# Optimization experiments

Measured on AMD Instinct MI355X. Metric: run time of the kernel, lower is better.

## Reference

```python
import jax, jax.numpy as jnp
import numpy as np
import math

N_VERT = 35709
N_FACE = 70789
BATCH = 32


def _normalize(x, axis=-1, eps=1e-12):
    n = jnp.linalg.norm(x, axis=axis, keepdims=True)
    return x / jnp.maximum(n, eps)


def setup_inputs() -> dict:
    key = jax.random.key(0)
    ks = jax.random.split(key, 9)
    coeff = jax.random.normal(ks[0], (BATCH, 277), jnp.float32)
    idBase = jax.random.normal(ks[1], (3 * N_VERT, 80), jnp.float32)
    exBase = jax.random.normal(ks[2], (3 * N_VERT, 64), jnp.float32)
    texBase = jax.random.normal(ks[3], (3 * N_VERT, 100), jnp.float32)
    meanshape = jax.random.normal(ks[4], (3 * N_VERT,), jnp.float32)
    meantex = jax.random.normal(ks[5], (3 * N_VERT,), jnp.float32)
    face_buf = jax.random.randint(ks[6], (N_FACE, 3), 0, N_VERT, jnp.int32)
    # point_buf may index the appended zero-normal row at position N_FACE (padding)
    point_buf = jax.random.randint(ks[7], (N_VERT, 8), 0, N_FACE + 1, jnp.int32)
    keypoints = jax.random.randint(ks[8], (68,), 0, N_VERT, jnp.int32)
    return dict(coeff=coeff, idBase=idBase, exBase=exBase, texBase=texBase,
                meanshape=meanshape, meantex=meantex, face_buf=face_buf,
                point_buf=point_buf, keypoints=keypoints)


def reference(coeff, idBase, exBase, texBase, meanshape, meantex,
              face_buf, point_buf, keypoints):
    B = coeff.shape[0]
    # ---- Split_coeff (canonical 80/64/100/3/27/3 layout) ----
    id_c = coeff[:, :80]
    ex_c = coeff[:, 80:144]
    tex_c = coeff[:, 144:244]
    angles = coeff[:, 244:247]
    gamma = coeff[:, 247:274]
    trans = coeff[:, 274:277]
    cam_scale = jnp.ones((B, 1), coeff.dtype)
    f_scale = jnp.ones((B, 1), coeff.dtype)

    # ---- Shape formation ----
    fs = (jnp.einsum('ij,aj->ai', idBase, id_c)
          + jnp.einsum('ij,aj->ai', exBase, ex_c)
          + meanshape[None, :])
    fs = fs.reshape(B, -1, 3)  # [B, N, 3]
    fs = fs - jnp.mean(meanshape.reshape(-1, 3), axis=0)[None, None, :]

    # ---- Texture formation ----
    tex = (jnp.einsum('ij,aj->ai', texBase, tex_c) + meantex[None, :]).reshape(B, -1, 3)

    # ---- Rotation matrix (Rz @ Ry @ Rx, then transpose) ----
    cx, sx = jnp.cos(angles[:, 0]), jnp.sin(angles[:, 0])
    cy, sy = jnp.cos(angles[:, 1]), jnp.sin(angles[:, 1])
    cz, sz = jnp.cos(angles[:, 2]), jnp.sin(angles[:, 2])
    o, z = jnp.ones_like(cx), jnp.zeros_like(cx)
    Rx = jnp.stack([o, z, z, z, cx, -sx, z, sx, cx], -1).reshape(B, 3, 3)
    Ry = jnp.stack([cy, z, sy, z, o, z, -sy, z, cy], -1).reshape(B, 3, 3)
    Rz = jnp.stack([cz, -sz, z, sz, cz, z, z, z, o], -1).reshape(B, 3, 3)
    rot = jnp.swapaxes(jnp.matmul(jnp.matmul(Rz, Ry), Rx), 1, 2)  # [B,3,3]

    # ---- Compute_norm: gather face verts, cross, aggregate to vertices ----
    v1 = fs[:, face_buf[:, 0], :]  # [B, F, 3]
    v2 = fs[:, face_buf[:, 1], :]
    v3 = fs[:, face_buf[:, 2], :]
    face_norm = _normalize(jnp.cross(v1 - v2, v2 - v3), axis=2)  # [B, F, 3]
    face_norm = jnp.concatenate(
        [face_norm, jnp.zeros((B, 1, 3), face_norm.dtype)], axis=1)  # pad row
    v_norm = _normalize(jnp.sum(face_norm[:, point_buf, :], axis=2), axis=2)  # [B,N,3]

    norm_r = jnp.matmul(v_norm, rot)

    # ---- Rigid transform + landmarks ----
    fst = jnp.matmul(fs, rot) + trans[:, None, :]
    lm = fst[:, keypoints, :]  # [B, 68, 3]

    # ---- Projection block (applied to landmarks) ----
    focal = 1015.0 * f_scale  # [B,1]
    camera_pos = jnp.array([0.0, 0.0, 10.0], coeff.dtype) * cam_scale[:, :, None]  # [B,1,3]
    reverse_z = jnp.diag(jnp.array([1.0, 1.0, -1.0], coeff.dtype))
    z1 = jnp.zeros((B, 1), coeff.dtype)
    z2 = jnp.zeros((B, 2), coeff.dtype)
    o1 = jnp.ones((B, 1), coeff.dtype)
    p_matrix = jnp.concatenate(
        [focal, z1, 112.0 * o1, z1, focal, 112.0 * o1, z2, o1], axis=1).reshape(B, 3, 3)
    lm_cam = jnp.matmul(lm, reverse_z[None]) + camera_pos
    aug = jnp.matmul(lm_cam, jnp.swapaxes(p_matrix, 1, 2))
    landmark_p = aug[..., :2] / aug[..., 2:3]

    # ---- SH illumination ----
    init_lit = jnp.array([0.8, 0, 0, 0, 0, 0, 0, 0, 0], coeff.dtype)
    g = gamma.reshape(B, 3, 9) + init_lit[None, None, :]
    pi = math.pi
    a0, a1, a2 = pi, 2 * pi / math.sqrt(3.0), 2 * pi / math.sqrt(8.0)
    c0 = 1.0 / math.sqrt(4 * pi)
    c1 = math.sqrt(3.0) / math.sqrt(4 * pi)
    c2 = 3 * math.sqrt(5.0) / math.sqrt(12 * pi)
    nx, ny, nz = norm_r[..., 0], norm_r[..., 1], norm_r[..., 2]
    Y = jnp.stack([
        a0 * c0 * jnp.ones_like(nx),
        -a1 * c1 * ny,
        a1 * c1 * nz,
        -a1 * c1 * nx,
        a2 * c2 * nx * ny,
        -a2 * c2 * ny * nz,
        a2 * c2 * 0.5 / math.sqrt(3.0) * (3 * nz * nz - 1),
        -a2 * c2 * nx * nz,
        a2 * c2 * 0.5 * (nx * nx - ny * ny),
    ], axis=-1)  # [B, N, 9]
    lighting = jnp.einsum('bnk,bck->bnc', Y, g)  # [B, N, 3]
    face_color = tex * lighting

    return face_color, landmark_p, fst
```

## Files before the change

kernel.cpp:

```cpp
#include <hip/hip_runtime.h>

#define N_VERT 35709
#define N_FACE 70789
#define NB 32
#define M3 (3*N_VERT)

#define WS_FS4X  ((size_t)0)
#define WS_FN4X  (WS_FS4X + (size_t)N_VERT*128)
#define WS_CPAD  (WS_FN4X + (size_t)(N_FACE+1)*128)
#define WS_ROT   (WS_CPAD + (size_t)NB*256)
#define WS_TRE   (WS_ROT + (size_t)NB*9)
#define WS_G     (WS_TRE + (size_t)NB*3)
#define WS_MEAN  (WS_G + (size_t)NB*27)

#define FC_OFF   ((size_t)0)
#define LM_OFF   ((size_t)NB*M3)
#define FST_OFF  (LM_OFF + (size_t)NB*68*2)

#define A0C0 0.88622692545275801f
#define A1C1 1.77245385090551603f
#define A2C2 2.42703239430f
#define Y6C  0.70062393935f
#define Y8C  1.21351619715f

__global__ void __launch_bounds__(256) face3d_stageA1(
    const float* __restrict__ ms, float* __restrict__ ws) {
  float s0=0.f, s1=0.f, s2=0.f;
  for (int v = blockIdx.x*256 + threadIdx.x; v < N_VERT; v += gridDim.x*256) {
    s0 += ms[3*v+0]; s1 += ms[3*v+1]; s2 += ms[3*v+2];
  }
  #pragma unroll
  for (int off = 32; off > 0; off >>= 1) {
    s0 += __shfl_down(s0, off);
    s1 += __shfl_down(s1, off);
    s2 += __shfl_down(s2, off);
  }
  if ((threadIdx.x & 63) == 0) {
    atomicAdd(&ws[WS_MEAN+0], s0);
    atomicAdd(&ws[WS_MEAN+1], s1);
    atomicAdd(&ws[WS_MEAN+2], s2);
  }
}

__global__ void __launch_bounds__(256) face3d_stageA2(
    const float* __restrict__ coeff, float* __restrict__ ws) {
  int t = threadIdx.x;
  float m0 = ws[WS_MEAN+0]*(1.0f/N_VERT);
  float m1 = ws[WS_MEAN+1]*(1.0f/N_VERT);
  float m2 = ws[WS_MEAN+2]*(1.0f/N_VERT);
  for (int idx = t; idx < NB*256; idx += 256) {
    int b = idx >> 8, k = idx & 255;
    ws[WS_CPAD + idx] = (k < 244) ? coeff[b*277 + k] : 0.0f;
  }
  for (int idx = t; idx < NB*27; idx += 256) {
    int b = idx / 27, k = idx - b*27;
    ws[WS_G + idx] = coeff[b*277 + 247 + k] + (((k % 9) == 0) ? 0.8f : 0.0f);
  }
  if (t < NB) {
    int b = t;
    float ax = coeff[b*277+244], ay = coeff[b*277+245], az = coeff[b*277+246];
    float cx=cosf(ax), sx=sinf(ax);
    float cy=cosf(ay), sy=sinf(ay);
    float cz=cosf(az), sz=sinf(az);
    float T00=cz*cy, T01=-sz, T02=cz*sy;
    float T10=sz*cy, T11=cz,  T12=sz*sy;
    float T20=-sy,   T21=0.f, T22=cy;
    float R[3][3];
    R[0][0]=T00; R[0][1]=T01*cx+T02*sx; R[0][2]=-T01*sx+T02*cx;
    R[1][0]=T10; R[1][1]=T11*cx+T12*sx; R[1][2]=-T11*sx+T12*cx;
    R[2][0]=T20; R[2][1]=T21*cx+T22*sx; R[2][2]=-T21*sx+T22*cx;
    float rot[3][3];
    #pragma unroll
    for (int c=0;c<3;c++)
      #pragma unroll
      for (int j=0;j<3;j++)
        rot[c][j] = R[j][c];
    #pragma unroll
    for (int c=0;c<3;c++)
      #pragma unroll
      for (int j=0;j<3;j++)
        ws[WS_ROT + b*9 + c*3 + j] = rot[c][j];
    #pragma unroll
    for (int j=0;j<3;j++)
      ws[WS_TRE + b*3 + j] = coeff[b*277+274+j]
        - (m0*rot[0][j] + m1*rot[1][j] + m2*rot[2][j]);
  }
}

template<int NK4, int COFF>
__device__ __forceinline__ void phaseK(const float* __restrict__ Arow,
                                       const float4* __restrict__ Wl,
                                       float* __restrict__ acc) {
  const float4* __restrict__ A = (const float4*)Arow;
  float4 cur = A[0];
  #pragma unroll 1
  for (int s = 0; s < NK4; ++s) {
    float4 a = cur;
    if (s + 1 < NK4) cur = A[s+1];
    #pragma unroll
    for (int b = 0; b < NB; ++b) {
      float4 w = Wl[b*64 + COFF + s];
      acc[b] = fmaf(a.x, w.x, fmaf(a.y, w.y, fmaf(a.z, w.z, fmaf(a.w, w.w, acc[b]))));
    }
  }
}

__global__ void __launch_bounds__(256) face3d_stageB(
    const float* __restrict__ idB, const float* __restrict__ exB,
    const float* __restrict__ texB, const float* __restrict__ meanshape,
    const float* __restrict__ meantex, const float* __restrict__ cpad,
    float* __restrict__ fs4x, float* __restrict__ texOut) {
  __shared__ float4 W[2048];
  int t = threadIdx.x;
  {
    const float4* __restrict__ src = (const float4*)cpad;
    #pragma unroll
    for (int j = 0; j < 8; ++j) W[t + 256*j] = src[t + 256*j];
  }
  __syncthreads();
  int r = blockIdx.x*256 + t;
  if (r >= M3) return;

  float acc[NB];
  #pragma unroll
  for (int b=0;b<NB;b++) acc[b]=0.f;
  phaseK<20, 0 >(idB + (size_t)r*80,  W, acc);
  phaseK<16, 20>(exB + (size_t)r*64,  W, acc);
  {
    float ms = meanshape[r];
    int v = r/3, c = r - 3*v;
    float* dst = fs4x + (size_t)v*128 + c;
    #pragma unroll
    for (int b=0;b<NB;b++) dst[b*4] = acc[b] + ms;
  }
  #pragma unroll
  for (int b=0;b<NB;b++) acc[b]=0.f;
  phaseK<25, 36>(texB + (size_t)r*100, W, acc);
  {
    float mt = meantex[r];
    #pragma unroll
    for (int b=0;b<NB;b++) texOut[(size_t)b*M3 + r] = acc[b] + mt;
  }
}

__global__ void __launch_bounds__(256) face3d_stageC(
    const int* __restrict__ face_buf, const float* __restrict__ fs4x,
    float* __restrict__ fn4x) {
  int t = threadIdx.x;
  int b = t & 31, fi = t >> 5;
  int f = blockIdx.x*8 + fi;
  if (f > N_FACE) return;
  float4* o = (float4*)(fn4x + ((size_t)f*32 + b)*4);
  if (f == N_FACE) { *o = make_float4(0.f,0.f,0.f,0.f); return; }
  int i0 = face_buf[f*3+0];
  int i1 = face_buf[f*3+1];
  int i2 = face_buf[f*3+2];
  float4 p1 = *(const float4*)(fs4x + ((size_t)i0*32 + b)*4);
  float4 p2 = *(const float4*)(fs4x + ((size_t)i1*32 + b)*4);
  float4 p3 = *(const float4*)(fs4x + ((size_t)i2*32 + b)*4);
  float e1x = p1.x-p2.x, e1y = p1.y-p2.y, e1z = p1.z-p2.z;
  float e2x = p2.x-p3.x, e2y = p2.y-p3.y, e2z = p2.z-p3.z;
  float nx = e1y*e2z - e1z*e2y;
  float ny = e1z*e2x - e1x*e2z;
  float nz = e1x*e2y - e1y*e2x;
  float inv = 1.0f / fmaxf(sqrtf(nx*nx + ny*ny + nz*nz), 1e-12f);
  *o = make_float4(nx*inv, ny*inv, nz*inv, 0.f);
}

__global__ void __launch_bounds__(256) face3d_stageD(
    const int* __restrict__ point_buf, const int* __restrict__ keypoints,
    const float* __restrict__ fs4x, const float* __restrict__ fn4x,
    const float* __restrict__ rotAll, const float* __restrict__ treAll,
    const float* __restrict__ gAll, float* __restrict__ out) {
  const int mainBlocks = (N_VERT + 7)/8;
  int bid = blockIdx.x;
  int t = threadIdx.x;
  if (bid < mainBlocks) {
    __shared__ float rotL[NB*9];
    __shared__ float treL[NB*3];
    __shared__ float gL[NB*27];
    __shared__ float fstL[NB*33];
    __shared__ float LL[NB*33];
    if (t < NB*9)  rotL[t] = rotAll[t];
    if (t < NB*3)  treL[t] = treAll[t];
    for (int i = t; i < NB*27; i += 256) gL[i] = gAll[i];
    __syncthreads();
    int b = t & 31, vi = t >> 5;
    int v0 = bid*8;
    int v = v0 + vi;
    if (v < N_VERT) {
      const int4 pb0 = *(const int4*)(point_buf + (size_t)v*8);
      const int4 pb1 = *(const int4*)(point_buf + (size_t)v*8 + 4);
      float4 g0 = *(const float4*)(fn4x + ((size_t)pb0.x*32 + b)*4);
      float4 g1 = *(const float4*)(fn4x + ((size_t)pb0.y*32 + b)*4);
      float4 g2 = *(const float4*)(fn4x + ((size_t)pb0.z*32 + b)*4);
      float4 g3 = *(const float4*)(fn4x + ((size_t)pb0.w*32 + b)*4);
      float4 g4 = *(const float4*)(fn4x + ((size_t)pb1.x*32 + b)*4);
      float4 g5 = *(const float4*)(fn4x + ((size_t)pb1.y*32 + b)*4);
      float4 g6 = *(const float4*)(fn4x + ((size_t)pb1.z*32 + b)*4);
      float4 g7 = *(const float4*)(fn4x + ((size_t)pb1.w*32 + b)*4);
      float sx = ((g0.x+g1.x)+(g2.x+g3.x)) + ((g4.x+g5.x)+(g6.x+g7.x));
      float sy = ((g0.y+g1.y)+(g2.y+g3.y)) + ((g4.y+g5.y)+(g6.y+g7.y));
      float sz = ((g0.z+g1.z)+(g2.z+g3.z)) + ((g4.z+g5.z)+(g6.z+g7.z));
      float inv = 1.0f / fmaxf(sqrtf(sx*sx + sy*sy + sz*sz), 1e-12f);
      float n0 = sx*inv, n1 = sy*inv, n2 = sz*inv;
      const float* rot = rotL + b*9;
      float r00=rot[0], r01=rot[1], r02=rot[2];
      float r10=rot[3], r11=rot[4], r12=rot[5];
      float r20=rot[6], r21=rot[7], r22=rot[8];
      float nx = n0*r00 + n1*r10 + n2*r20;
      float ny = n0*r01 + n1*r11 + n2*r21;
      float nz = n0*r02 + n1*r12 + n2*r22;
      float Y1 = -A1C1*ny;
      float Y2 =  A1C1*nz;
      float Y3 = -A1C1*nx;
      float Y4 =  A2C2*nx*ny;
      float Y5 = -A2C2*ny*nz;
      float Y6 =  Y6C*(3.f*nz*nz - 1.f);
      float Y7 = -A2C2*nx*nz;
      float Y8 =  Y8C*(nx*nx - ny*ny);
      const float* g = gL + b*27;
      #pragma unroll
      for (int c = 0; c < 3; ++c) {
        const float* gc = g + c*9;
        float Lc = A0C0*gc[0] + Y1*gc[1] + Y2*gc[2] + Y3*gc[3] + Y4*gc[4]
                 + Y5*gc[5] + Y6*gc[6] + Y7*gc[7] + Y8*gc[8];
        LL[b*33 + vi*4 + c] = Lc;
      }
      float4 fsv = *(const float4*)(fs4x + ((size_t)v*32 + b)*4);
      const float* tre = treL + b*3;
      fstL[b*33 + vi*4 + 0] = fsv.x*r00 + fsv.y*r10 + fsv.z*r20 + tre[0];
      fstL[b*33 + vi*4 + 1] = fsv.x*r01 + fsv.y*r11 + fsv.z*r21 + tre[1];
      fstL[b*33 + vi*4 + 2] = fsv.x*r02 + fsv.y*r12 + fsv.z*r22 + tre[2];
    }
    __syncthreads();
    int b2 = t >> 3, w = t & 7;
    if (v0 + w < N_VERT) {
      size_t obase = (size_t)b2*M3 + (size_t)(v0 + w)*3;
      float f0 = fstL[b2*33 + w*4 + 0];
      float f1 = fstL[b2*33 + w*4 + 1];
      float f2 = fstL[b2*33 + w*4 + 2];
      out[FST_OFF + obase + 0] = f0;
      out[FST_OFF + obase + 1] = f1;
      out[FST_OFF + obase + 2] = f2;
      float l0 = LL[b2*33 + w*4 + 0];
      float l1 = LL[b2*33 + w*4 + 1];
      float l2 = LL[b2*33 + w*4 + 2];
      float t0 = out[FC_OFF + obase + 0];
      float t1 = out[FC_OFF + obase + 1];
      float t2 = out[FC_OFF + obase + 2];
      out[FC_OFF + obase + 0] = t0*l0;
      out[FC_OFF + obase + 1] = t1*l1;
      out[FC_OFF + obase + 2] = t2*l2;
    }
  } else {
    int idx = (bid - mainBlocks)*256 + t;
    if (idx >= NB*68) return;
    int b = idx & 31, j = idx >> 5;
    int kp = keypoints[j];
    const float* rot = rotAll + b*9;
    const float* tre = treAll + b*3;
    float4 fsv = *(const float4*)(fs4x + ((size_t)kp*32 + b)*4);
    float o0 = fsv.x*rot[0] + fsv.y*rot[3] + fsv.z*rot[6] + tre[0];
    float o1 = fsv.x*rot[1] + fsv.y*rot[4] + fsv.z*rot[7] + tre[1];
    float o2 = fsv.x*rot[2] + fsv.y*rot[5] + fsv.z*rot[8] + tre[2];
    float zc = 10.0f - o2;
    float axv = 1015.0f*o0 + 112.0f*zc;
    float ayv = 1015.0f*o1 + 112.0f*zc;
    out[LM_OFF + (size_t)b*136 + (size_t)j*2 + 0] = axv/zc;
    out[LM_OFF + (size_t)b*136 + (size_t)j*2 + 1] = ayv/zc;
  }
}

extern "C" void kernel_launch(void* const* d_in, const int* in_sizes, int n_in,
                              void* d_out, int out_size, void* d_ws, size_t ws_size,
                              hipStream_t stream) {
  const float* coeff     = (const float*)d_in[0];
  const float* idB       = (const float*)d_in[1];
  const float* exB       = (const float*)d_in[2];
  const float* texB      = (const float*)d_in[3];
  const float* meanshape = (const float*)d_in[4];
  const float* meantex   = (const float*)d_in[5];
  const int*   face_buf  = (const int*)d_in[6];
  const int*   point_buf = (const int*)d_in[7];
  const int*   keypoints = (const int*)d_in[8];
  float* out = (float*)d_out;
  float* ws  = (float*)d_ws;

  hipMemsetAsync((char*)d_ws + WS_MEAN*sizeof(float), 0, 3*sizeof(float), stream);

  hipLaunchKernelGGL(face3d_stageA1, dim3(56), dim3(256), 0, stream, meanshape, ws);
  hipLaunchKernelGGL(face3d_stageA2, dim3(1), dim3(256), 0, stream, coeff, ws);

  int gridB = (M3 + 255)/256;
  hipLaunchKernelGGL(face3d_stageB, dim3(gridB), dim3(256), 0, stream,
                     idB, exB, texB, meanshape, meantex,
                     ws + WS_CPAD, ws + WS_FS4X, out + FC_OFF);

  int gridC = (N_FACE + 1 + 7)/8;
  hipLaunchKernelGGL(face3d_stageC, dim3(gridC), dim3(256), 0, stream,
                     face_buf, ws + WS_FS4X, ws + WS_FN4X);

  int mainBlocks = (N_VERT + 7)/8;
  int lmBlocks   = (NB*68 + 255)/256;
  hipLaunchKernelGGL(face3d_stageD, dim3(mainBlocks + lmBlocks), dim3(256), 0, stream,
                     point_buf, keypoints, ws + WS_FS4X, ws + WS_FN4X,
                     ws + WS_ROT, ws + WS_TRE, ws + WS_G, out);
}
```

Baseline: 290.1 us.

## Register-tile basis GEMV 8x8 and split workspace into batch-group slabs

Result: slower. 312.2 us (+7.6%).

```diff
diff --git a/kernel.cpp b/kernel.cpp
--- a/kernel.cpp
+++ b/kernel.cpp
@@ -5,23 +5,33 @@
 #define NB 32
 #define M3 (3*N_VERT)
 
-#define WS_FS4X  ((size_t)0)
-#define WS_FN4X  (WS_FS4X + (size_t)N_VERT*128)
-#define WS_CPAD  (WS_FN4X + (size_t)(N_FACE+1)*128)
-#define WS_ROT   (WS_CPAD + (size_t)NB*256)
-#define WS_TRE   (WS_ROT + (size_t)NB*9)
-#define WS_G     (WS_TRE + (size_t)NB*3)
-#define WS_MEAN  (WS_G + (size_t)NB*27)
-
-#define FC_OFF   ((size_t)0)
-#define LM_OFF   ((size_t)NB*M3)
-#define FST_OFF  (LM_OFF + (size_t)NB*68*2)
+#define FSS ((size_t)N_VERT*16)
+#define FNS ((size_t)(N_FACE+1)*16)
+
+#define WS_FS   ((size_t)0)
+#define WS_FN   (WS_FS + 8*FSS)
+#define WS_CPAD (WS_FN + 8*FNS)
+#define WS_ROT  (WS_CPAD + (size_t)NB*256)
+#define WS_TRE  (WS_ROT + (size_t)NB*9)
+#define WS_G    (WS_TRE + (size_t)NB*3)
+#define WS_MEAN (WS_G + (size_t)NB*27)
+
+#define FC_OFF  ((size_t)0)
+#define LM_OFF  ((size_t)NB*M3)
+#define FST_OFF (LM_OFF + (size_t)NB*68*2)
 
 #define A0C0 0.88622692545275801f
 #define A1C1 1.77245385090551603f
 #define A2C2 2.42703239430f
 #define Y6C  0.70062393935f
 #define Y8C  1.21351619715f
+
+typedef float vf4 __attribute__((ext_vector_type(4)));
+
+__device__ __forceinline__ void nt_store4(float* p, float a, float b, float c, float d) {
+  vf4 v = {a, b, c, d};
+  __builtin_nontemporal_store(v, (vf4*)p);
+}
 
 __global__ void __launch_bounds__(256) face3d_stageA1(
     const float* __restrict__ ms, float* __restrict__ ws) {
@@ -87,124 +97,170 @@
   }
 }
 
-template<int NK4, int COFF>
-__device__ __forceinline__ void phaseK(const float* __restrict__ Arow,
-                                       const float4* __restrict__ Wl,
-                                       float* __restrict__ acc) {
-  const float4* __restrict__ A = (const float4*)Arow;
-  float4 cur = A[0];
+template<int NK4, int KROW, int COFF>
+__device__ __forceinline__ void phase88(const float* __restrict__ A0,
+                                        int row0,
+                                        const float4* __restrict__ W,
+                                        int bg,
+                                        float acc[8][8]) {
+  const float4* p[8];
+  #pragma unroll
+  for (int i = 0; i < 8; ++i) {
+    int r = row0 + i; if (r >= M3) r = M3-1;
+    p[i] = (const float4*)(A0 + (size_t)r*KROW);
+  }
+  float4 cur[8];
+  #pragma unroll
+  for (int i = 0; i < 8; ++i) cur[i] = p[i][0];
   #pragma unroll 1
   for (int s = 0; s < NK4; ++s) {
-    float4 a = cur;
-    if (s + 1 < NK4) cur = A[s+1];
-    #pragma unroll
-    for (int b = 0; b < NB; ++b) {
-      float4 w = Wl[b*64 + COFF + s];
-      acc[b] = fmaf(a.x, w.x, fmaf(a.y, w.y, fmaf(a.z, w.z, fmaf(a.w, w.w, acc[b]))));
-    }
-  }
-}
-
-__global__ void __launch_bounds__(256) face3d_stageB(
+    float4 a[8];
+    #pragma unroll
+    for (int i = 0; i < 8; ++i) a[i] = cur[i];
+    if (s + 1 < NK4) {
+      #pragma unroll
+      for (int i = 0; i < 8; ++i) cur[i] = p[i][s+1];
+    }
+    #pragma unroll
+    for (int j = 0; j < 8; ++j) {
+      float4 w = W[(size_t)(bg + 4*j)*65 + COFF + s];
+      #pragma unroll
+      for (int i = 0; i < 8; ++i) {
+        acc[i][j] = fmaf(a[i].x, w.x, fmaf(a[i].y, w.y,
+                    fmaf(a[i].z, w.z, fmaf(a[i].w, w.w, acc[i][j]))));
+      }
+    }
+  }
+}
+
+__global__ void __launch_bounds__(256,1) face3d_stageB(
     const float* __restrict__ idB, const float* __restrict__ exB,
     const float* __restrict__ texB, const float* __restrict__ meanshape,
     const float* __restrict__ meantex, const float* __restrict__ cpad,
-    float* __restrict__ fs4x, float* __restrict__ texOut) {
-  __shared__ float4 W[2048];
+    float* __restrict__ fsS, float* __restrict__ texOut) {
+  __shared__ float4 W[32*65];
   int t = threadIdx.x;
   {
     const float4* __restrict__ src = (const float4*)cpad;
     #pragma unroll
-    for (int j = 0; j < 8; ++j) W[t + 256*j] = src[t + 256*j];
+    for (int n = 0; n < 8; ++n) {
+      int idx = t + 256*n;
+      int b = idx >> 6, k = idx & 63;
+      W[b*65 + k] = src[idx];
+    }
   }
   __syncthreads();
-  int r = blockIdx.x*256 + t;
-  if (r >= M3) return;
-
-  float acc[NB];
-  #pragma unroll
-  for (int b=0;b<NB;b++) acc[b]=0.f;
-  phaseK<20, 0 >(idB + (size_t)r*80,  W, acc);
-  phaseK<16, 20>(exB + (size_t)r*64,  W, acc);
-  {
-    float ms = meanshape[r];
-    int v = r/3, c = r - 3*v;
-    float* dst = fs4x + (size_t)v*128 + c;
-    #pragma unroll
-    for (int b=0;b<NB;b++) dst[b*4] = acc[b] + ms;
-  }
-  #pragma unroll
-  for (int b=0;b<NB;b++) acc[b]=0.f;
-  phaseK<25, 36>(texB + (size_t)r*100, W, acc);
-  {
-    float mt = meantex[r];
-    #pragma unroll
-    for (int b=0;b<NB;b++) texOut[(size_t)b*M3 + r] = acc[b] + mt;
+  int bg = t & 3;
+  int row0 = blockIdx.x*512 + (t >> 2)*8;
+  if (row0 >= M3) return;
+
+  float acc[8][8];
+  #pragma unroll
+  for (int i=0;i<8;i++)
+    #pragma unroll
+    for (int j=0;j<8;j++) acc[i][j]=0.f;
+
+  phase88<20, 80, 0 >(idB, row0, W, bg, acc);
+  phase88<16, 64, 20>(exB, row0, W, bg, acc);
+
+  #pragma unroll
+  for (int i = 0; i < 8; ++i) {
+    int r = row0 + i;
+    if (r < M3) {
+      float msv = meanshape[r];
+      int v = r/3, c = r - 3*v;
+      float* dst = fsS + (size_t)v*16 + bg*4 + c;
+      #pragma unroll
+      for (int j = 0; j < 8; ++j)
+        dst[j*FSS] = acc[i][j] + msv;
+    }
+  }
+
+  #pragma unroll
+  for (int i=0;i<8;i++)
+    #pragma unroll
+    for (int j=0;j<8;j++) acc[i][j]=0.f;
+
+  phase88<25, 100, 36>(texB, row0, W, bg, acc);
+
+  #pragma unroll
+  for (int i = 0; i < 8; ++i) {
+    int r = row0 + i;
+    if (r < M3) {
+      float mtv = meantex[r];
+      #pragma unroll
+      for (int j = 0; j < 8; ++j) {
+        int b = bg + 4*j;
+        __builtin_nontemporal_store(acc[i][j] + mtv, &texOut[(size_t)b*M3 + r]);
+      }
+    }
   }
 }
 
 __global__ void __launch_bounds__(256) face3d_stageC(
-    const int* __restrict__ face_buf, const float* __restrict__ fs4x,
-    float* __restrict__ fn4x) {
+    const int* __restrict__ face_buf, const float* __restrict__ fsS,
+    float* __restrict__ fnS) {
   int t = threadIdx.x;
-  int b = t & 31, fi = t >> 5;
-  int f = blockIdx.x*8 + fi;
+  int bg = blockIdx.x & 7;
+  int f = (blockIdx.x >> 3)*64 + (t >> 2);
+  int bsub = t & 3;
   if (f > N_FACE) return;
-  float4* o = (float4*)(fn4x + ((size_t)f*32 + b)*4);
-  if (f == N_FACE) { *o = make_float4(0.f,0.f,0.f,0.f); return; }
+  float* o = fnS + bg*FNS + (size_t)f*16 + bsub*4;
+  if (f == N_FACE) {
+    nt_store4(o, 0.f, 0.f, 0.f, 0.f);
+    return;
+  }
   int i0 = face_buf[f*3+0];
   int i1 = face_buf[f*3+1];
   int i2 = face_buf[f*3+2];
-  float4 p1 = *(const float4*)(fs4x + ((size_t)i0*32 + b)*4);
-  float4 p2 = *(const float4*)(fs4x + ((size_t)i1*32 + b)*4);
-  float4 p3 = *(const float4*)(fs4x + ((size_t)i2*32 + b)*4);
+  const float* fs = fsS + bg*FSS + bsub*4;
+  float4 p1 = *(const float4*)(fs + (size_t)i0*16);
+  float4 p2 = *(const float4*)(fs + (size_t)i1*16);
+  float4 p3 = *(const float4*)(fs + (size_t)i2*16);
   float e1x = p1.x-p2.x, e1y = p1.y-p2.y, e1z = p1.z-p2.z;
   float e2x = p2.x-p3.x, e2y = p2.y-p3.y, e2z = p2.z-p3.z;
   float nx = e1y*e2z - e1z*e2y;
   float ny = e1z*e2x - e1x*e2z;
   float nz = e1x*e2y - e1y*e2x;
   float inv = 1.0f / fmaxf(sqrtf(nx*nx + ny*ny + nz*nz), 1e-12f);
-  *o = make_float4(nx*inv, ny*inv, nz*inv, 0.f);
-}
-
+  nt_store4(o, nx*inv, ny*inv, nz*inv, 0.f);
+}
+
+#define DVB 558
 __global__ void __launch_bounds__(256) face3d_stageD(
     const int* __restrict__ point_buf, const int* __restrict__ keypoints,
-    const float* __restrict__ fs4x, const float* __restrict__ fn4x,
+    const float* __restrict__ fsS, const float* __restrict__ fnS,
     const float* __restrict__ rotAll, const float* __restrict__ treAll,
     const float* __restrict__ gAll, float* __restrict__ out) {
-  const int mainBlocks = (N_VERT + 7)/8;
+  const int mainBlocks = 8*DVB;
   int bid = blockIdx.x;
   int t = threadIdx.x;
   if (bid < mainBlocks) {
-    __shared__ float rotL[NB*9];
-    __shared__ float treL[NB*3];
-    __shared__ float gL[NB*27];
-    __shared__ float fstL[NB*33];
-    __shared__ float LL[NB*33];
-    if (t < NB*9)  rotL[t] = rotAll[t];
-    if (t < NB*3)  treL[t] = treAll[t];
-    for (int i = t; i < NB*27; i += 256) gL[i] = gAll[i];
-    __syncthreads();
-    int b = t & 31, vi = t >> 5;
-    int v0 = bid*8;
+    __shared__ float fstL[4*193];
+    __shared__ float LL[4*193];
+    int bg = bid & 7;
+    int v0 = (bid >> 3)*64;
+    int bsub = t & 3, vi = t >> 2;
     int v = v0 + vi;
+    int b = bg*4 + bsub;
     if (v < N_VERT) {
       const int4 pb0 = *(const int4*)(point_buf + (size_t)v*8);
       const int4 pb1 = *(const int4*)(point_buf + (size_t)v*8 + 4);
-      float4 g0 = *(const float4*)(fn4x + ((size_t)pb0.x*32 + b)*4);
-      float4 g1 = *(const float4*)(fn4x + ((size_t)pb0.y*32 + b)*4);
-      float4 g2 = *(const float4*)(fn4x + ((size_t)pb0.z*32 + b)*4);
-      float4 g3 = *(const float4*)(fn4x + ((size_t)pb0.w*32 + b)*4);
-      float4 g4 = *(const float4*)(fn4x + ((size_t)pb1.x*32 + b)*4);
-      float4 g5 = *(const float4*)(fn4x + ((size_t)pb1.y*32 + b)*4);
-      float4 g6 = *(const float4*)(fn4x + ((size_t)pb1.z*32 + b)*4);
-      float4 g7 = *(const float4*)(fn4x + ((size_t)pb1.w*32 + b)*4);
+      const float* fn = fnS + bg*FNS + bsub*4;
+      float4 g0 = *(const float4*)(fn + (size_t)pb0.x*16);
+      float4 g1 = *(const float4*)(fn + (size_t)pb0.y*16);
+      float4 g2 = *(const float4*)(fn + (size_t)pb0.z*16);
+      float4 g3 = *(const float4*)(fn + (size_t)pb0.w*16);
+      float4 g4 = *(const float4*)(fn + (size_t)pb1.x*16);
+      float4 g5 = *(const float4*)(fn + (size_t)pb1.y*16);
+      float4 g6 = *(const float4*)(fn + (size_t)pb1.z*16);
+      float4 g7 = *(const float4*)(fn + (size_t)pb1.w*16);
       float sx = ((g0.x+g1.x)+(g2.x+g3.x)) + ((g4.x+g5.x)+(g6.x+g7.x));
       float sy = ((g0.y+g1.y)+(g2.y+g3.y)) + ((g4.y+g5.y)+(g6.y+g7.y));
       float sz = ((g0.z+g1.z)+(g2.z+g3.z)) + ((g4.z+g5.z)+(g6.z+g7.z));
       float inv = 1.0f / fmaxf(sqrtf(sx*sx + sy*sy + sz*sz), 1e-12f);
       float n0 = sx*inv, n1 = sy*inv, n2 = sz*inv;
-      const float* rot = rotL + b*9;
+      const float* rot = rotAll + b*9;
       float r00=rot[0], r01=rot[1], r02=rot[2];
       float r10=rot[3], r11=rot[4], r12=rot[5];
       float r20=rot[6], r21=rot[7], r22=rot[8];
@@ -219,39 +275,33 @@
       float Y6 =  Y6C*(3.f*nz*nz - 1.f);
       float Y7 = -A2C2*nx*nz;
       float Y8 =  Y8C*(nx*nx - ny*ny);
-      const float* g = gL + b*27;
+      const float* g = gAll + b*27;
       #pragma unroll
       for (int c = 0; c < 3; ++c) {
         const float* gc = g + c*9;
-        float Lc = A0C0*gc[0] + Y1*gc[1] + Y2*gc[2] + Y3*gc[3] + Y4*gc[4]
-                 + Y5*gc[5] + Y6*gc[6] + Y7*gc[7] + Y8*gc[8];
-        LL[b*33 + vi*4 + c] = Lc;
+        LL[bsub*193 + vi*3 + c] =
+            A0C0*gc[0] + Y1*gc[1] + Y2*gc[2] + Y3*gc[3] + Y4*gc[4]
+          + Y5*gc[5] + Y6*gc[6] + Y7*gc[7] + Y8*gc[8];
       }
-      float4 fsv = *(const float4*)(fs4x + ((size_t)v*32 + b)*4);
-      const float* tre = treL + b*3;
-      fstL[b*33 + vi*4 + 0] = fsv.x*r00 + fsv.y*r10 + fsv.z*r20 + tre[0];
-      fstL[b*33 + vi*4 + 1] = fsv.x*r01 + fsv.y*r11 + fsv.z*r21 + tre[1];
-      fstL[b*33 + vi*4 + 2] = fsv.x*r02 + fsv.y*r12 + fsv.z*r22 + tre[2];
+      float4 fsv = *(const float4*)(fsS + bg*FSS + (size_t)v*16 + bsub*4);
+      const float* tre = treAll + b*3;
+      fstL[bsub*193 + vi*3 + 0] = fsv.x*r00 + fsv.y*r10 + fsv.z*r20 + tre[0];
+      fstL[bsub*193 + vi*3 + 1] = fsv.x*r01 + fsv.y*r11 + fsv.z*r21 + tre[1];
+      fstL[bsub*193 + vi*3 + 2] = fsv.x*r02 + fsv.y*r12 + fsv.z*r22 + tre[2];
     }
     __syncthreads();
-    int b2 = t >> 3, w = t & 7;
+    int b2 = t >> 6, w = t & 63;
     if (v0 + w < N_VERT) {
-      size_t obase = (size_t)b2*M3 + (size_t)(v0 + w)*3;
-      float f0 = fstL[b2*33 + w*4 + 0];
-      float f1 = fstL[b2*33 + w*4 + 1];
-      float f2 = fstL[b2*33 + w*4 + 2];
-      out[FST_OFF + obase + 0] = f0;
-      out[FST_OFF + obase + 1] = f1;
-      out[FST_OFF + obase + 2] = f2;
-      float l0 = LL[b2*33 + w*4 + 0];
-      float l1 = LL[b2*33 + w*4 + 1];
-      float l2 = LL[b2*33 + w*4 + 2];
-      float t0 = out[FC_OFF + obase + 0];
-      float t1 = out[FC_OFF + obase + 1];
-      float t2 = out[FC_OFF + obase + 2];
-      out[FC_OFF + obase + 0] = t0*l0;
-      out[FC_OFF + obase + 1] = t1*l1;
-      out[FC_OFF + obase + 2] = t2*l2;
+      int bb = bg*4 + b2;
+      size_t obase = (size_t)bb*M3 + (size_t)(v0 + w)*3;
+      #pragma unroll
+      for (int c = 0; c < 3; ++c)
+        __builtin_nontemporal_store(fstL[b2*193 + w*3 + c], &out[FST_OFF + obase + c]);
+      #pragma unroll
+      for (int c = 0; c < 3; ++c) {
+        float tx = out[FC_OFF + obase + c];
+        __builtin_nontemporal_store(tx*LL[b2*193 + w*3 + c], &out[FC_OFF + obase + c]);
+      }
     }
   } else {
     int idx = (bid - mainBlocks)*256 + t;
@@ -260,15 +310,15 @@
     int kp = keypoints[j];
     const float* rot = rotAll + b*9;
     const float* tre = treAll + b*3;
-    float4 fsv = *(const float4*)(fs4x + ((size_t)kp*32 + b)*4);
+    float4 fsv = *(const float4*)(fsS + (size_t)(b>>2)*FSS + (size_t)kp*16 + (b&3)*4);
     float o0 = fsv.x*rot[0] + fsv.y*rot[3] + fsv.z*rot[6] + tre[0];
     float o1 = fsv.x*rot[1] + fsv.y*rot[4] + fsv.z*rot[7] + tre[1];
     float o2 = fsv.x*rot[2] + fsv.y*rot[5] + fsv.z*rot[8] + tre[2];
     float zc = 10.0f - o2;
     float axv = 1015.0f*o0 + 112.0f*zc;
     float ayv = 1015.0f*o1 + 112.0f*zc;
-    out[LM_OFF + (size_t)b*136 + (size_t)j*2 + 0] = axv/zc;
-    out[LM_OFF + (size_t)b*136 + (size_t)j*2 + 1] = ayv/zc;
+    __builtin_nontemporal_store(axv/zc, &out[LM_OFF + (size_t)b*136 + (size_t)j*2 + 0]);
+    __builtin_nontemporal_store(ayv/zc, &out[LM_OFF + (size_t)b*136 + (size_t)j*2 + 1]);
   }
 }
 
@@ -287,23 +337,23 @@
   float* out = (float*)d_out;
   float* ws  = (float*)d_ws;
 
-  hipMemsetAsync((char*)d_ws + WS_MEAN*sizeof(float), 0, 3*sizeof(float), stream);
+  (void)hipMemsetAsync((char*)d_ws + WS_MEAN*sizeof(float), 0, 3*sizeof(float), stream);
 
   hipLaunchKernelGGL(face3d_stageA1, dim3(56), dim3(256), 0, stream, meanshape, ws);
   hipLaunchKernelGGL(face3d_stageA2, dim3(1), dim3(256), 0, stream, coeff, ws);
 
-  int gridB = (M3 + 255)/256;
+  int gridB = (M3 + 511)/512;
   hipLaunchKernelGGL(face3d_stageB, dim3(gridB), dim3(256), 0, stream,
                      idB, exB, texB, meanshape, meantex,
-                     ws + WS_CPAD, ws + WS_FS4X, out + FC_OFF);
-
-  int gridC = (N_FACE + 1 + 7)/8;
+                     ws + WS_CPAD, ws + WS_FS, out + FC_OFF);
+
+  int gridC = 8 * ((N_FACE + 1 + 63)/64);
   hipLaunchKernelGGL(face3d_stageC, dim3(gridC), dim3(256), 0, stream,
-                     face_buf, ws + WS_FS4X, ws + WS_FN4X);
-
-  int mainBlocks = (N_VERT + 7)/8;
+                     face_buf, ws + WS_FS, ws + WS_FN);
+
+  int mainBlocks = 8*DVB;
   int lmBlocks   = (NB*68 + 255)/256;
   hipLaunchKernelGGL(face3d_stageD, dim3(mainBlocks + lmBlocks), dim3(256), 0, stream,
-                     point_buf, keypoints, ws + WS_FS4X, ws + WS_FN4X,
+                     point_buf, keypoints, ws + WS_FS, ws + WS_FN,
                      ws + WS_ROT, ws + WS_TRE, ws + WS_G, out);
 }
```
